# Performance work log

Measured on AMD Instinct MI355X. Metric: run time of the kernel, lower is better.

## Reference

```python
import jax, jax.numpy as jnp
import numpy as np

CLIP_LIMIT = 40.0
GRID = (8, 8)
NUM_BINS = 256


def setup_inputs() -> dict:
    key = jax.random.key(0)
    # CLAHE expects image values in [0, 1]
    x = jax.random.uniform(key, (8, 3, 1024, 1024), dtype=jnp.float32)
    return {"x": x}


def _interp_coords(n_tiles, tile_size, length):
    """Per-pixel tile-pair indices and blend weight along one axis.

    Follows kornia's half-tile interpolation grid: pixels in the first/last
    half-tile use only the nearest tile LUT; interior pixels blend the two
    nearest tile LUTs with weights linear over a full tile span (denom 2*half-1).
    """
    half = tile_size // 2
    pos = jnp.arange(length)
    j = pos // half          # interpolation-tile row/col index (0 .. 2*n_tiles-1)
    p = pos % half           # offset within the half tile
    r0 = jnp.clip((j - 1) // 2, 0, n_tiles - 1)
    r1 = jnp.clip(r0 + 1, 0, n_tiles - 1)
    denom = float(2 * half - 1)
    w = jnp.where(j % 2 == 1, (2 * half - 1) - p, (half - 1) - p).astype(jnp.float32) / denom
    w = jnp.where(j == 0, 1.0, w)  # first half-tile: nearest LUT only
    return r0, r1, w


def _clahe(x):
    B, C, H, W = x.shape
    GH, GW = GRID
    th = -(-H // GH); th += th % 2   # even tile height (kornia even_tile_size=True)
    tw = -(-W // GW); tw += tw % 2
    Hp, Wp = th * GH, tw * GW
    xp = jnp.pad(x, ((0, 0), (0, 0), (0, Hp - H), (0, Wp - W)), mode='reflect') if (Hp > H or Wp > W) else x

    # tiles: B x C x GH x GW x th x tw
    tiles = xp.reshape(B, C, GH, th, GW, tw).transpose(0, 1, 2, 4, 3, 5)
    pixels = th * tw
    T = B * C * GH * GW

    # per-tile 256-bin histogram (histc over [0,1] -> floor(x*256), last bin closed)
    bins = jnp.clip((tiles * NUM_BINS).astype(jnp.int32), 0, NUM_BINS - 1).reshape(T, pixels)
    hist = jnp.zeros((T, NUM_BINS), jnp.float32).at[jnp.arange(T)[:, None], bins].add(1.0)

    # clip + uniform redistribution of the excess (kornia scheme)
    if CLIP_LIMIT > 0:
        max_val = max(CLIP_LIMIT * pixels // NUM_BINS, 1.0)
        hist = jnp.minimum(hist, max_val)
        clipped = pixels - hist.sum(axis=1)                 # excess per tile
        residual = jnp.mod(clipped, NUM_BINS)
        hist = hist + ((clipped - residual) / NUM_BINS)[:, None]
        hist = hist + (jnp.arange(NUM_BINS)[None, :] < residual[:, None]).astype(jnp.float32)

    # LUT from CDF, floored to emulate integer conversion
    lut_scale = (NUM_BINS - 1) / pixels
    lut = jnp.floor(jnp.clip(jnp.cumsum(hist, axis=1) * lut_scale, 0, NUM_BINS - 1))
    lut = lut.reshape(B, C, GH, GW, NUM_BINS)

    # per-pixel LUT lookup index (kornia uses (x*255).long())
    idx = jnp.clip((xp * 255.0).astype(jnp.int32), 0, 255)

    r0, r1, wy = _interp_coords(GH, th, Hp)
    c0, c1, wx = _interp_coords(GW, tw, Wp)

    b_i = jnp.arange(B)[:, None, None, None]
    ch_i = jnp.arange(C)[None, :, None, None]

    def g(ry, cx):
        # gather lut[b, c, ry(y), cx(x), idx[b,c,y,x]] -> (B, C, Hp, Wp)
        return lut[b_i, ch_i, ry[None, None, :, None], cx[None, None, None, :], idx]

    wy2 = wy[:, None]
    wx2 = wx[None, :]
    out = (wy2 * wx2 * g(r0, c0)
           + wy2 * (1.0 - wx2) * g(r0, c1)
           + (1.0 - wy2) * wx2 * g(r1, c0)
           + (1.0 - wy2) * (1.0 - wx2) * g(r1, c1))
    return out[..., :H, :W] / 255.0


def reference(x):
    return _clahe(x)
```

## Files before the change

kernel.cpp:

```cpp
#include <hip/hip_runtime.h>

#define NBINS 256
#define TILE  128
#define CLIPV 2560u

typedef float  fx4 __attribute__((ext_vector_type(4)));
typedef float  fx2 __attribute__((ext_vector_type(2)));

__global__ __launch_bounds__(256) void clahe_hist_lut(
        const float* __restrict__ x, float* __restrict__ lut) {
    const int t   = blockIdx.x;
    const int tid = threadIdx.x;

    __shared__ unsigned int hs[NBINS * 8];
    __shared__ int          scan[2][NBINS];
    __shared__ unsigned int wsum[4];

    #pragma unroll
    for (int k = 0; k < 8; ++k) hs[k * NBINS + tid] = 0u;
    __syncthreads();

    const int tx = t & 7;
    const int ty = (t >> 3) & 7;
    const int bc = t >> 6;
    const float* base = x + ((size_t)bc * 1024 + (size_t)ty * TILE) * 1024
                          + (size_t)tx * TILE;

    const int sub    = tid & 7;
    const int lane32 = tid & 31;
    const int rgrp   = tid >> 5;
    #pragma unroll 4
    for (int rr = 0; rr < 16; ++rr) {
        const int row = rr * 8 + rgrp;
        const fx4 v = __builtin_nontemporal_load(
            (const fx4*)(base + (size_t)row * 1024 + lane32 * 4));
        int b0 = min(max((int)(v.x * 256.0f), 0), 255);
        int b1 = min(max((int)(v.y * 256.0f), 0), 255);
        int b2 = min(max((int)(v.z * 256.0f), 0), 255);
        int b3 = min(max((int)(v.w * 256.0f), 0), 255);
        atomicAdd(&hs[b0 * 8 + sub], 1u);
        atomicAdd(&hs[b1 * 8 + sub], 1u);
        atomicAdd(&hs[b2 * 8 + sub], 1u);
        atomicAdd(&hs[b3 * 8 + sub], 1u);
    }
    __syncthreads();

    const uint4* hp = (const uint4*)(&hs[tid * 8]);
    const uint4 ha = hp[0], hb = hp[1];
    const unsigned int total = ha.x + ha.y + ha.z + ha.w
                             + hb.x + hb.y + hb.z + hb.w;
    const unsigned int hv = min(total, CLIPV);
    unsigned int e = total - hv;
    #pragma unroll
    for (int off = 32; off > 0; off >>= 1) e += __shfl_down(e, off, 64);
    if ((tid & 63) == 0) wsum[tid >> 6] = e;
    __syncthreads();
    const unsigned int E        = wsum[0] + wsum[1] + wsum[2] + wsum[3];
    const unsigned int add      = E >> 8;
    const unsigned int residual = E & 255u;
    const int h2 = (int)(hv + add + ((unsigned)tid < residual ? 1u : 0u));

    scan[0][tid] = h2;
    __syncthreads();
    int src = 0;
    #pragma unroll
    for (int off = 1; off < 256; off <<= 1) {
        int v = scan[src][tid];
        if (tid >= off) v += scan[src][tid - off];
        scan[src ^ 1][tid] = v;
        __syncthreads();
        src ^= 1;
    }
    const int cum = scan[src][tid];
    const float l = fminf((float)cum * (255.0f / 16384.0f), 255.0f);
    lut[(size_t)t * NBINS + tid] = floorf(l);
}

__global__ __launch_bounds__(256) void clahe_apply(
        const float* __restrict__ x, const float* __restrict__ lut,
        float* __restrict__ out) {
    __shared__ fx4 l01s[1024];

    const int blk = blockIdx.x;
    const int bc  = blk >> 6;
    const int rg  = blk & 63;
    const int y0  = rg * 16;
    const int tid = threadIdx.x;

    const int j = y0 >> 6;
    int r0 = (j - 1) >> 1;
    r0 = min(max(r0, 0), 7);
    const int r1 = min(r0 + 1, 7);

    {
        const float* lb = lut + (size_t)bc * 64 * NBINS;
        const fx4* s0 = (const fx4*)(lb + (size_t)r0 * 8 * NBINS);
        const fx4* s1 = (const fx4*)(lb + (size_t)r1 * 8 * NBINS);
        #pragma unroll
        for (int e = 0; e < 2; ++e) {
            const int i4 = e * 256 + tid;
            const fx4 a = s0[i4];
            const fx4 b = s1[i4];
            l01s[i4 * 2]     = (fx4){a.x, b.x, a.y, b.y};
            l01s[i4 * 2 + 1] = (fx4){a.z, b.z, a.w, b.w};
        }
    }
    __syncthreads();
    const fx2* lv = (const fx2*)l01s;

    int o0k[4], o1k[4];
    float wxk[4];
    #pragma unroll
    for (int k = 0; k < 4; ++k) {
        const int xx = tid * 4 + k;
        const int jc = xx >> 6, pc = xx & 63;
        int c0 = (jc - 1) >> 1;
        c0 = min(max(c0, 0), 7);
        o0k[k] = c0 * NBINS;
        o1k[k] = min(c0 + 1, 7) * NBINS;
        wxk[k] = (jc == 0) ? 1.0f
               : (float)((jc & 1) ? (127 - pc) : (63 - pc)) / 127.0f;
    }

    const bool jzero = (j == 0);
    const bool jodd  = (j & 1);
    const size_t rowbase = ((size_t)bc * 1024 + (size_t)y0) * 1024 + tid * 4;

    #pragma unroll 4
    for (int r = 0; r < 16; ++r) {
        const int p = (y0 + r) & 63;
        const float wy = jzero ? 1.0f
                       : (float)(jodd ? (127 - p) : (63 - p)) / 127.0f;

        const fx4 v = __builtin_nontemporal_load(
            (const fx4*)(x + rowbase + (size_t)r * 1024));
        const float vv[4] = {v.x, v.y, v.z, v.w};
        float res[4];
        #pragma unroll
        for (int k = 0; k < 4; ++k) {
            const int idx = min(max((int)(vv[k] * 255.0f), 0), 255);
            const fx2 G0 = lv[o0k[k] + idx];
            const fx2 G1 = lv[o1k[k] + idx];
            const float wx = wxk[k];
            const float a = fmaf(wx, G0.x - G1.x, G1.x);
            const float b = fmaf(wx, G0.y - G1.y, G1.y);
            res[k] = fmaf(wy, a - b, b) * (1.0f / 255.0f);
        }
        const fx4 o4 = {res[0], res[1], res[2], res[3]};
        __builtin_nontemporal_store(
            o4, (fx4*)(out + rowbase + (size_t)r * 1024));
    }
}

extern "C" void kernel_launch(void* const* d_in, const int* in_sizes, int n_in,
                              void* d_out, int out_size, void* d_ws, size_t ws_size,
                              hipStream_t stream) {
    const float* x = (const float*)d_in[0];
    float* out = (float*)d_out;
    float* lut = (float*)d_ws;

    clahe_hist_lut<<<1536, 256, 0, stream>>>(x, lut);
    clahe_apply<<<24 * 64, 256, 0, stream>>>(x, lut, out);
}
```

Before: 190.0 us.

## Precompute packed byte LUT indices in histogram pass and pack LUT as uint8

The histogram kernel now also computes each pixel's LUT index and writes it as packed bytes to workspace. The apply kernel reads these bytes instead of re-reading the float input, which reduces global read traffic. LUTs are stored as uint8, and the shared table packs the four neighbouring tile LUT values into one word, so each pixel needs a single LDS lookup. The cost is an extra global write of indices in the first pass, plus reliance on a larger workspace region.

Measured after the change: 179.4 us. -5.5%, faster.

```diff
diff --git a/kernel.cpp b/kernel.cpp
--- a/kernel.cpp
+++ b/kernel.cpp
@@ -4,11 +4,13 @@
 #define TILE  128
 #define CLIPV 2560u
 
-typedef float  fx4 __attribute__((ext_vector_type(4)));
-typedef float  fx2 __attribute__((ext_vector_type(2)));
+typedef float fx4 __attribute__((ext_vector_type(4)));
+
+#define IDX_OFF (512 * 1024)
 
 __global__ __launch_bounds__(256) void clahe_hist_lut(
-        const float* __restrict__ x, float* __restrict__ lut) {
+        const float* __restrict__ x, unsigned char* __restrict__ lut8,
+        unsigned int* __restrict__ idxw) {
     const int t   = blockIdx.x;
     const int tid = threadIdx.x;
 
@@ -23,8 +25,9 @@
     const int tx = t & 7;
     const int ty = (t >> 3) & 7;
     const int bc = t >> 6;
-    const float* base = x + ((size_t)bc * 1024 + (size_t)ty * TILE) * 1024
-                          + (size_t)tx * TILE;
+    const size_t pbase = ((size_t)bc * 1024 + (size_t)ty * TILE) * 1024
+                       + (size_t)tx * TILE;
+    const float* base = x + pbase;
 
     const int sub    = tid & 7;
     const int lane32 = tid & 31;
@@ -34,14 +37,20 @@
         const int row = rr * 8 + rgrp;
         const fx4 v = __builtin_nontemporal_load(
             (const fx4*)(base + (size_t)row * 1024 + lane32 * 4));
-        int b0 = min(max((int)(v.x * 256.0f), 0), 255);
-        int b1 = min(max((int)(v.y * 256.0f), 0), 255);
-        int b2 = min(max((int)(v.z * 256.0f), 0), 255);
-        int b3 = min(max((int)(v.w * 256.0f), 0), 255);
+        const int b0 = min(max((int)(v.x * 256.0f), 0), 255);
+        const int b1 = min(max((int)(v.y * 256.0f), 0), 255);
+        const int b2 = min(max((int)(v.z * 256.0f), 0), 255);
+        const int b3 = min(max((int)(v.w * 256.0f), 0), 255);
         atomicAdd(&hs[b0 * 8 + sub], 1u);
         atomicAdd(&hs[b1 * 8 + sub], 1u);
         atomicAdd(&hs[b2 * 8 + sub], 1u);
         atomicAdd(&hs[b3 * 8 + sub], 1u);
+        const unsigned i0 = (unsigned)min(max((int)(v.x * 255.0f), 0), 255);
+        const unsigned i1 = (unsigned)min(max((int)(v.y * 255.0f), 0), 255);
+        const unsigned i2 = (unsigned)min(max((int)(v.z * 255.0f), 0), 255);
+        const unsigned i3 = (unsigned)min(max((int)(v.w * 255.0f), 0), 255);
+        idxw[(pbase + (size_t)row * 1024 + lane32 * 4) >> 2] =
+            i0 | (i1 << 8) | (i2 << 16) | (i3 << 24);
     }
     __syncthreads();
 
@@ -73,13 +82,14 @@
     }
     const int cum = scan[src][tid];
     const float l = fminf((float)cum * (255.0f / 16384.0f), 255.0f);
-    lut[(size_t)t * NBINS + tid] = floorf(l);
+    lut8[(size_t)t * NBINS + tid] = (unsigned char)floorf(l);
 }
 
 __global__ __launch_bounds__(256) void clahe_apply(
-        const float* __restrict__ x, const float* __restrict__ lut,
+        const unsigned int* __restrict__ idxr,
+        const unsigned char* __restrict__ lut8,
         float* __restrict__ out) {
-    __shared__ fx4 l01s[1024];
+    __shared__ unsigned int ptab[8 * NBINS];
 
     const int blk = blockIdx.x;
     const int bc  = blk >> 6;
@@ -93,22 +103,24 @@
     const int r1 = min(r0 + 1, 7);
 
     {
-        const float* lb = lut + (size_t)bc * 64 * NBINS;
-        const fx4* s0 = (const fx4*)(lb + (size_t)r0 * 8 * NBINS);
-        const fx4* s1 = (const fx4*)(lb + (size_t)r1 * 8 * NBINS);
+        const unsigned char* L0 = lut8 + (size_t)bc * 64 * NBINS + (size_t)r0 * 8 * NBINS;
+        const unsigned char* L1 = lut8 + (size_t)bc * 64 * NBINS + (size_t)r1 * 8 * NBINS;
+        unsigned a0[8], a1[8];
         #pragma unroll
-        for (int e = 0; e < 2; ++e) {
-            const int i4 = e * 256 + tid;
-            const fx4 a = s0[i4];
-            const fx4 b = s1[i4];
-            l01s[i4 * 2]     = (fx4){a.x, b.x, a.y, b.y};
-            l01s[i4 * 2 + 1] = (fx4){a.z, b.z, a.w, b.w};
+        for (int c = 0; c < 8; ++c) {
+            a0[c] = L0[c * NBINS + tid];
+            a1[c] = L1[c * NBINS + tid];
+        }
+        #pragma unroll
+        for (int c0 = 0; c0 < 8; ++c0) {
+            const int c1 = min(c0 + 1, 7);
+            ptab[c0 * NBINS + tid] =
+                a0[c0] | (a0[c1] << 8) | (a1[c0] << 16) | (a1[c1] << 24);
         }
     }
     __syncthreads();
-    const fx2* lv = (const fx2*)l01s;
 
-    int o0k[4], o1k[4];
+    int ock[4];
     float wxk[4];
     #pragma unroll
     for (int k = 0; k < 4; ++k) {
@@ -116,8 +128,7 @@
         const int jc = xx >> 6, pc = xx & 63;
         int c0 = (jc - 1) >> 1;
         c0 = min(max(c0, 0), 7);
-        o0k[k] = c0 * NBINS;
-        o1k[k] = min(c0 + 1, 7) * NBINS;
+        ock[k] = c0 * NBINS;
         wxk[k] = (jc == 0) ? 1.0f
                : (float)((jc & 1) ? (127 - pc) : (63 - pc)) / 127.0f;
     }
@@ -132,18 +143,19 @@
         const float wy = jzero ? 1.0f
                        : (float)(jodd ? (127 - p) : (63 - p)) / 127.0f;
 
-        const fx4 v = __builtin_nontemporal_load(
-            (const fx4*)(x + rowbase + (size_t)r * 1024));
-        const float vv[4] = {v.x, v.y, v.z, v.w};
+        const unsigned pk = idxr[(rowbase + (size_t)r * 1024) >> 2];
         float res[4];
         #pragma unroll
         for (int k = 0; k < 4; ++k) {
-            const int idx = min(max((int)(vv[k] * 255.0f), 0), 255);
-            const fx2 G0 = lv[o0k[k] + idx];
-            const fx2 G1 = lv[o1k[k] + idx];
+            const unsigned id = (pk >> (8 * k)) & 0xffu;
+            const unsigned e = ptab[ock[k] + id];
+            const float g00 = (float)(e & 0xffu);
+            const float g01 = (float)((e >> 8) & 0xffu);
+            const float g10 = (float)((e >> 16) & 0xffu);
+            const float g11 = (float)(e >> 24);
             const float wx = wxk[k];
-            const float a = fmaf(wx, G0.x - G1.x, G1.x);
-            const float b = fmaf(wx, G0.y - G1.y, G1.y);
+            const float a = fmaf(wx, g00 - g01, g01);
+            const float b = fmaf(wx, g10 - g11, g11);
             res[k] = fmaf(wy, a - b, b) * (1.0f / 255.0f);
         }
         const fx4 o4 = {res[0], res[1], res[2], res[3]};
@@ -157,8 +169,9 @@
                               hipStream_t stream) {
     const float* x = (const float*)d_in[0];
     float* out = (float*)d_out;
-    float* lut = (float*)d_ws;
+    unsigned char* lut8 = (unsigned char*)d_ws;
+    unsigned int*  idxw = (unsigned int*)((char*)d_ws + IDX_OFF);
 
-    clahe_hist_lut<<<1536, 256, 0, stream>>>(x, lut);
-    clahe_apply<<<24 * 64, 256, 0, stream>>>(x, lut, out);
+    clahe_hist_lut<<<1536, 256, 0, stream>>>(x, lut8, idxw);
+    clahe_apply<<<24 * 64, 256, 0, stream>>>(idxw, lut8, out);
 }
```
